# Optimization experiments

Measured on AMD Instinct MI355X. Metric: run time of the kernel, lower is better.

The kernel has to match this reference:

```python
import jax, jax.numpy as jnp
import numpy as np
from jax.scipy.special import logsumexp

EPSILON = 0.1
N_ITERS = 5


def setup_inputs() -> dict:
    key = jax.random.key(0)
    k1, k2, k3 = jax.random.split(key, 3)
    B, Q, T, D = 16, 1024, 1024, 256
    preds = jax.random.normal(k1, (B, Q, D), dtype=jnp.float32)
    targets = jax.random.normal(k2, (B, T, D), dtype=jnp.float32)
    filter = jax.random.normal(k3, (B, T), dtype=jnp.float32)
    return {"preds": preds, "targets": targets, "filter": filter}


def _cdist(x, y):
    x2 = jnp.sum(x * x, axis=-1)[:, :, None]          # [B,Q,1]
    y2 = jnp.sum(y * y, axis=-1)[:, None, :]          # [B,1,T]
    xy = jnp.einsum("bqd,btd->bqt", x, y)             # [B,Q,T]
    return jnp.sqrt(jnp.maximum(x2 + y2 - 2.0 * xy, 0.0))


def reference(preds, targets, filter):
    eps = EPSILON
    B, Q, _ = preds.shape
    T = targets.shape[1]
    cost = _cdist(preds, targets)                     # [B,Q,T]
    filter_cost = 2.0 * jnp.max(cost)
    cost = jnp.where(filter[:, None, :] <= 0, filter_cost, cost)
    u = jnp.zeros((B, Q), dtype=cost.dtype)
    v = jnp.zeros((B, T), dtype=cost.dtype)
    for _ in range(N_ITERS):
        u = -eps * logsumexp(-(cost - v[:, None, :]) / eps, axis=2)
        v = -eps * logsumexp(-(cost - u[:, :, None]) / eps, axis=1)
    P = jnp.exp((u[:, :, None] + v[:, None, :] - cost) / eps)
    idx_tgt = jnp.argmax(P, axis=2)
    return (idx_tgt, P)
```

## Files before the change

kernel.cpp:

```cpp
#include <hip/hip_runtime.h>
#include <math.h>

#define BB 16
#define QQ 1024
#define TT 1024
#define DD 256
#define EPS 0.1f
#define INV_EPS 10.0f
#define SINK_ITERS 5
#define FCONST 128.0f

typedef _Float16 f16;
typedef _Float16 f16x4 __attribute__((ext_vector_type(4)));
typedef _Float16 f16x8 __attribute__((ext_vector_type(8)));
typedef float f32x4 __attribute__((ext_vector_type(4)));

__global__ __launch_bounds__(256) void cvt_kernel(
    const float* __restrict__ preds, const float* __restrict__ targets,
    f16* __restrict__ Ahi, f16* __restrict__ Alo,
    f16* __restrict__ Bhi, f16* __restrict__ Blo,
    float* __restrict__ x2, float* __restrict__ y2)
{
  int w = threadIdx.x >> 6, l = threadIdx.x & 63;
  int row = blockIdx.x * 4 + w;
  const float* src; f16 *hi, *lo; float* nrm;
  if (row < BB*QQ) {
    src = preds + (size_t)row * DD;
    hi = Ahi + (size_t)row * DD; lo = Alo + (size_t)row * DD; nrm = x2 + row;
  } else {
    int r = row - BB*QQ;
    src = targets + (size_t)r * DD;
    hi = Bhi + (size_t)r * DD; lo = Blo + (size_t)r * DD; nrm = y2 + r;
  }
  float4 v = ((const float4*)src)[l];
  f16x4 h, lw;
  h.x = (f16)v.x; h.y = (f16)v.y; h.z = (f16)v.z; h.w = (f16)v.w;
  lw.x = (f16)(v.x - (float)h.x); lw.y = (f16)(v.y - (float)h.y);
  lw.z = (f16)(v.z - (float)h.z); lw.w = (f16)(v.w - (float)h.w);
  *(f16x4*)(hi + l*4) = h;
  *(f16x4*)(lo + l*4) = lw;
  float s = v.x*v.x + v.y*v.y + v.z*v.z + v.w*v.w;
  #pragma unroll
  for (int o = 32; o; o >>= 1) s += __shfl_down(s, o, 64);
  if (l == 0) *nrm = s;
}

__global__ __launch_bounds__(256) void cost_mfma_kernel(
    const f16* __restrict__ Ahi, const f16* __restrict__ Alo,
    const f16* __restrict__ Bhi, const f16* __restrict__ Blo,
    const float* __restrict__ x2, const float* __restrict__ y2,
    const float* __restrict__ filter,
    float* __restrict__ cost, float* __restrict__ costT, int useT)
{
  __shared__ f16 sA[2][128*32];
  __shared__ f16 sB[2][128*32];
  int b = blockIdx.z;
  int q0 = blockIdx.y * 128, t0 = blockIdx.x * 128;
  int tid = threadIdx.x, w = tid >> 6, l = tid & 63;
  int rq = (w >> 1) * 64, rt = (w & 1) * 64;
  int fr = l & 15, fg = l >> 4;
  const f16* pA[2] = { Ahi + ((size_t)b*QQ + q0) * DD, Alo + ((size_t)b*QQ + q0) * DD };
  const f16* pB[2] = { Bhi + ((size_t)b*TT + t0) * DD, Blo + ((size_t)b*TT + t0) * DD };
  f32x4 acc[4][4] = {};
  for (int k0 = 0; k0 < DD; k0 += 32) {
    __syncthreads();
#if __has_builtin(__builtin_amdgcn_global_load_lds)
    #pragma unroll
    for (int j = 0; j < 2; ++j) {
      int chunk = w*128 + j*64 + l;
      int row = chunk >> 2, kc = chunk & 3;
      size_t go = (size_t)row * DD + k0 + kc*8;
      int lb = (w*128 + j*64) * 8;
      #pragma unroll
      for (int h = 0; h < 2; ++h) {
        __builtin_amdgcn_global_load_lds(
            (const __attribute__((address_space(1))) void*)(pA[h] + go),
            (__attribute__((address_space(3))) void*)&sA[h][lb], 16, 0, 0);
        __builtin_amdgcn_global_load_lds(
            (const __attribute__((address_space(1))) void*)(pB[h] + go),
            (__attribute__((address_space(3))) void*)&sB[h][lb], 16, 0, 0);
      }
    }
#else
    #pragma unroll
    for (int j = 0; j < 2; ++j) {
      int chunk = w*128 + j*64 + l;
      int row = chunk >> 2, kc = chunk & 3;
      size_t go = (size_t)row * DD + k0 + kc*8;
      #pragma unroll
      for (int h = 0; h < 2; ++h) {
        *(f16x8*)&sA[h][chunk*8] = *(const f16x8*)(pA[h] + go);
        *(f16x8*)&sB[h][chunk*8] = *(const f16x8*)(pB[h] + go);
      }
    }
#endif
    __syncthreads();
    f16x8 ah[4], al[4], bh[4], bl[4];
    #pragma unroll
    for (int f = 0; f < 4; ++f) {
      int ao = (rq + f*16 + fr)*32 + fg*8;
      ah[f] = *(const f16x8*)&sA[0][ao];
      al[f] = *(const f16x8*)&sA[1][ao];
      int bo = (rt + f*16 + fr)*32 + fg*8;
      bh[f] = *(const f16x8*)&sB[0][bo];
      bl[f] = *(const f16x8*)&sB[1][bo];
    }
    #pragma unroll
    for (int fm = 0; fm < 4; ++fm)
      #pragma unroll
      for (int fn = 0; fn < 4; ++fn) {
        acc[fm][fn] = __builtin_amdgcn_mfma_f32_16x16x32_f16(ah[fm], bh[fn], acc[fm][fn], 0, 0, 0);
        acc[fm][fn] = __builtin_amdgcn_mfma_f32_16x16x32_f16(ah[fm], bl[fn], acc[fm][fn], 0, 0, 0);
        acc[fm][fn] = __builtin_amdgcn_mfma_f32_16x16x32_f16(al[fm], bh[fn], acc[fm][fn], 0, 0, 0);
      }
  }
  float xv[16];
  #pragma unroll
  for (int fm = 0; fm < 4; ++fm)
    #pragma unroll
    for (int r = 0; r < 4; ++r)
      xv[fm*4+r] = x2[(size_t)b*QQ + q0 + rq + fm*16 + fg*4 + r];
  float yv[4], fv[4];
  #pragma unroll
  for (int fn = 0; fn < 4; ++fn) {
    int t = t0 + rt + fn*16 + fr;
    yv[fn] = y2[(size_t)b*TT + t];
    fv[fn] = filter[(size_t)b*TT + t];
  }
  #pragma unroll
  for (int fm = 0; fm < 4; ++fm) {
    #pragma unroll
    for (int fn = 0; fn < 4; ++fn) {
      int t = t0 + rt + fn*16 + fr;
      float cvr[4];
      #pragma unroll
      for (int r = 0; r < 4; ++r) {
        float c2 = xv[fm*4+r] + yv[fn] - 2.0f*acc[fm][fn][r];
        float c = sqrtf(fmaxf(c2, 0.f));
        if (fv[fn] <= 0.f) c = FCONST;
        cvr[r] = c;
        int q = q0 + rq + fm*16 + fg*4 + r;
        cost[((size_t)b*QQ + q)*TT + t] = c;
      }
      if (useT) {
        float* dst = costT + ((size_t)b*TT + t)*QQ + q0 + rq + fm*16 + fg*4;
        *(float4*)dst = make_float4(cvr[0], cvr[1], cvr[2], cvr[3]);
      }
    }
  }
}

__global__ __launch_bounds__(64) void norms_kernel(
    const float* __restrict__ preds, const float* __restrict__ targets,
    float* __restrict__ x2, float* __restrict__ y2)
{
  int row = blockIdx.x;
  const float* src; float* dst;
  if (row < BB*QQ) { src = preds + (size_t)row * DD; dst = x2 + row; }
  else { int r = row - BB*QQ; src = targets + (size_t)r * DD; dst = y2 + r; }
  float4 v = ((const float4*)src)[threadIdx.x];
  float s = v.x*v.x + v.y*v.y + v.z*v.z + v.w*v.w;
  #pragma unroll
  for (int o = 32; o; o >>= 1) s += __shfl_down(s, o, 64);
  if (threadIdx.x == 0) *dst = s;
}

#define LDSTR 132
__global__ __launch_bounds__(256) void cost_fp32_kernel(
    const float* __restrict__ preds, const float* __restrict__ targets,
    const float* __restrict__ x2, const float* __restrict__ y2,
    const float* __restrict__ filter,
    float* __restrict__ cost, float* __restrict__ costT, int useT)
{
  __shared__ float As[16*LDSTR];
  __shared__ float Bs[16*LDSTR];
  int b  = blockIdx.z;
  int q0 = blockIdx.y * 128;
  int t0 = blockIdx.x * 128;
  const float* Ab = preds   + ((size_t)b*QQ + q0) * DD;
  const float* Bb = targets + ((size_t)b*TT + t0) * DD;
  int tid = threadIdx.x;
  int srow = tid >> 2, sq = (tid & 3) << 2;
  int w = tid >> 6, l = tid & 63;
  int rq = ((w >> 1) << 6) + ((l >> 3) << 3);
  int rt = ((w & 1) << 6) + ((l & 7) << 3);
  float acc[8][8] = {};
  for (int k0 = 0; k0 < DD; k0 += 16) {
    float4 a0 = *(const float4*)(Ab + (size_t)srow*DD + k0 + sq);
    float4 a1 = *(const float4*)(Ab + (size_t)(srow+64)*DD + k0 + sq);
    float4 b0 = *(const float4*)(Bb + (size_t)srow*DD + k0 + sq);
    float4 b1 = *(const float4*)(Bb + (size_t)(srow+64)*DD + k0 + sq);
    __syncthreads();
    As[(sq+0)*LDSTR + srow] = a0.x; As[(sq+1)*LDSTR + srow] = a0.y;
    As[(sq+2)*LDSTR + srow] = a0.z; As[(sq+3)*LDSTR + srow] = a0.w;
    As[(sq+0)*LDSTR + srow+64] = a1.x; As[(sq+1)*LDSTR + srow+64] = a1.y;
    As[(sq+2)*LDSTR + srow+64] = a1.z; As[(sq+3)*LDSTR + srow+64] = a1.w;
    Bs[(sq+0)*LDSTR + srow] = b0.x; Bs[(sq+1)*LDSTR + srow] = b0.y;
    Bs[(sq+2)*LDSTR + srow] = b0.z; Bs[(sq+3)*LDSTR + srow] = b0.w;
    Bs[(sq+0)*LDSTR + srow+64] = b1.x; Bs[(sq+1)*LDSTR + srow+64] = b1.y;
    Bs[(sq+2)*LDSTR + srow+64] = b1.z; Bs[(sq+3)*LDSTR + srow+64] = b1.w;
    __syncthreads();
    #pragma unroll
    for (int k = 0; k < 16; ++k) {
      float4 af0 = *(const float4*)&As[k*LDSTR + rq];
      float4 af1 = *(const float4*)&As[k*LDSTR + rq + 4];
      float4 bf0 = *(const float4*)&Bs[k*LDSTR + rt];
      float4 bf1 = *(const float4*)&Bs[k*LDSTR + rt + 4];
      float aa[8] = {af0.x,af0.y,af0.z,af0.w,af1.x,af1.y,af1.z,af1.w};
      float bb[8] = {bf0.x,bf0.y,bf0.z,bf0.w,bf1.x,bf1.y,bf1.z,bf1.w};
      #pragma unroll
      for (int i = 0; i < 8; ++i)
        #pragma unroll
        for (int j = 0; j < 8; ++j)
          acc[i][j] = fmaf(aa[i], bb[j], acc[i][j]);
    }
  }
  float xq[8], yt[8], fvv[8];
  #pragma unroll
  for (int i = 0; i < 8; ++i) xq[i] = x2[(size_t)b*QQ + q0 + rq + i];
  #pragma unroll
  for (int j = 0; j < 8; ++j) {
    yt[j] = y2[(size_t)b*TT + t0 + rt + j];
    fvv[j] = filter[(size_t)b*TT + t0 + rt + j];
  }
  float cv[8][8];
  #pragma unroll
  for (int i = 0; i < 8; ++i)
    #pragma unroll
    for (int j = 0; j < 8; ++j) {
      float c2 = xq[i] + yt[j] - 2.f*acc[i][j];
      float c = sqrtf(fmaxf(c2, 0.f));
      if (fvv[j] <= 0.f) c = FCONST;
      cv[i][j] = c;
    }
  #pragma unroll
  for (int i = 0; i < 8; ++i) {
    float* dst = cost + ((size_t)b*QQ + q0 + rq + i) * TT + t0 + rt;
    *(float4*)dst       = make_float4(cv[i][0], cv[i][1], cv[i][2], cv[i][3]);
    *(float4*)(dst + 4) = make_float4(cv[i][4], cv[i][5], cv[i][6], cv[i][7]);
  }
  if (useT) {
    #pragma unroll
    for (int j = 0; j < 8; ++j) {
      float* dst = costT + ((size_t)b*TT + t0 + rt + j) * QQ + q0 + rq;
      *(float4*)dst       = make_float4(cv[0][j], cv[1][j], cv[2][j], cv[3][j]);
      *(float4*)(dst + 4) = make_float4(cv[4][j], cv[5][j], cv[6][j], cv[7][j]);
    }
  }
}

__device__ __forceinline__ float wave_max64(float v) {
  #pragma unroll
  for (int o = 1; o < 64; o <<= 1) v = fmaxf(v, __shfl_xor(v, o, 64));
  return v;
}
__device__ __forceinline__ float wave_sum64(float v) {
  #pragma unroll
  for (int o = 1; o < 64; o <<= 1) v += __shfl_xor(v, o, 64);
  return v;
}

__global__ __launch_bounds__(256) void u_kernel(
    const float* __restrict__ cost, const float* __restrict__ v, float* __restrict__ u)
{
  int row = (blockIdx.x << 2) + (threadIdx.x >> 6);
  int l = threadIdx.x & 63;
  int b = row >> 10;
  const float4* cr = (const float4*)(cost + (size_t)row * TT);
  const float4* vb = (const float4*)(v + (size_t)b * TT);
  float s[16], m = -3.0e38f;
  #pragma unroll
  for (int i = 0; i < 4; ++i) {
    float4 c4 = cr[l + (i << 6)];
    float4 v4 = vb[l + (i << 6)];
    s[4*i+0] = (v4.x - c4.x) * INV_EPS;
    s[4*i+1] = (v4.y - c4.y) * INV_EPS;
    s[4*i+2] = (v4.z - c4.z) * INV_EPS;
    s[4*i+3] = (v4.w - c4.w) * INV_EPS;
    m = fmaxf(m, fmaxf(fmaxf(s[4*i+0], s[4*i+1]), fmaxf(s[4*i+2], s[4*i+3])));
  }
  m = wave_max64(m);
  float sum = 0.f;
  #pragma unroll
  for (int i = 0; i < 16; ++i) sum += expf(s[i] - m);
  sum = wave_sum64(sum);
  if (l == 0) u[row] = -EPS * (m + logf(sum));
}

__global__ __launch_bounds__(256) void v_kernel(
    const float* __restrict__ cost, const float* __restrict__ costT, int useT,
    const float* __restrict__ filter, const float* __restrict__ u, float* __restrict__ v)
{
  int row = (blockIdx.x << 2) + (threadIdx.x >> 6);
  int l = threadIdx.x & 63;
  int b = row >> 10;
  int t = row & 1023;
  const float4* ub = (const float4*)(u + (size_t)b * QQ);
  bool filt = (filter[row] <= 0.f);
  float s[16], m = -3.0e38f;
  if (filt) {
    #pragma unroll
    for (int i = 0; i < 4; ++i) {
      float4 u4 = ub[l + (i << 6)];
      s[4*i+0] = (u4.x - FCONST) * INV_EPS;
      s[4*i+1] = (u4.y - FCONST) * INV_EPS;
      s[4*i+2] = (u4.z - FCONST) * INV_EPS;
      s[4*i+3] = (u4.w - FCONST) * INV_EPS;
      m = fmaxf(m, fmaxf(fmaxf(s[4*i+0], s[4*i+1]), fmaxf(s[4*i+2], s[4*i+3])));
    }
  } else if (useT) {
    const float4* cr = (const float4*)(costT + (size_t)row * QQ);
    #pragma unroll
    for (int i = 0; i < 4; ++i) {
      float4 u4 = ub[l + (i << 6)];
      float4 c4 = cr[l + (i << 6)];
      s[4*i+0] = (u4.x - c4.x) * INV_EPS;
      s[4*i+1] = (u4.y - c4.y) * INV_EPS;
      s[4*i+2] = (u4.z - c4.z) * INV_EPS;
      s[4*i+3] = (u4.w - c4.w) * INV_EPS;
      m = fmaxf(m, fmaxf(fmaxf(s[4*i+0], s[4*i+1]), fmaxf(s[4*i+2], s[4*i+3])));
    }
  } else {
    const float* cr = cost + (size_t)b*QQ*TT + t;
    #pragma unroll
    for (int i = 0; i < 4; ++i) {
      float4 u4 = ub[l + (i << 6)];
      int q = (l + (i << 6)) << 2;
      float c0 = cr[(size_t)(q+0) * TT];
      float c1 = cr[(size_t)(q+1) * TT];
      float c2 = cr[(size_t)(q+2) * TT];
      float c3 = cr[(size_t)(q+3) * TT];
      s[4*i+0] = (u4.x - c0) * INV_EPS;
      s[4*i+1] = (u4.y - c1) * INV_EPS;
      s[4*i+2] = (u4.z - c2) * INV_EPS;
      s[4*i+3] = (u4.w - c3) * INV_EPS;
      m = fmaxf(m, fmaxf(fmaxf(s[4*i+0], s[4*i+1]), fmaxf(s[4*i+2], s[4*i+3])));
    }
  }
  m = wave_max64(m);
  float sum = 0.f;
  #pragma unroll
  for (int i = 0; i < 16; ++i) sum += expf(s[i] - m);
  sum = wave_sum64(sum);
  if (l == 0) v[row] = -EPS * (m + logf(sum));
}

__global__ __launch_bounds__(256) void p_kernel(
    float* __restrict__ P, const float* __restrict__ u, const float* __restrict__ v,
    float* __restrict__ idxOut)
{
  int row = (blockIdx.x << 2) + (threadIdx.x >> 6);
  int l = threadIdx.x & 63;
  int b = row >> 10;
  float4* cr = (float4*)(P + (size_t)row * TT);
  const float4* vb = (const float4*)(v + (size_t)b * TT);
  float uu = u[row];
  float bestp = -1.f; int bestt = 0;
  #pragma unroll
  for (int i = 0; i < 4; ++i) {
    float4 c4 = cr[l + (i << 6)];
    float4 v4 = vb[l + (i << 6)];
    int t0 = (l + (i << 6)) << 2;
    float4 p4;
    p4.x = expf((uu + v4.x - c4.x) * INV_EPS);
    p4.y = expf((uu + v4.y - c4.y) * INV_EPS);
    p4.z = expf((uu + v4.z - c4.z) * INV_EPS);
    p4.w = expf((uu + v4.w - c4.w) * INV_EPS);
    if (p4.x > bestp) { bestp = p4.x; bestt = t0 + 0; }
    if (p4.y > bestp) { bestp = p4.y; bestt = t0 + 1; }
    if (p4.z > bestp) { bestp = p4.z; bestt = t0 + 2; }
    if (p4.w > bestp) { bestp = p4.w; bestt = t0 + 3; }
    cr[l + (i << 6)] = p4;
  }
  #pragma unroll
  for (int o = 1; o < 64; o <<= 1) {
    float op = __shfl_xor(bestp, o, 64);
    int   ot = __shfl_xor(bestt, o, 64);
    if (op > bestp || (op == bestp && ot < bestt)) { bestp = op; bestt = ot; }
  }
  if (l == 0) idxOut[row] = (float)bestt;
}

extern "C" void kernel_launch(void* const* d_in, const int* in_sizes, int n_in,
                              void* d_out, int out_size, void* d_ws, size_t ws_size,
                              hipStream_t stream) {
  const float* preds   = (const float*)d_in[0];
  const float* targets = (const float*)d_in[1];
  const float* filter  = (const float*)d_in[2];
  float* out = (float*)d_out;
  float* idxOut = out;
  float* P = out + (size_t)BB*QQ;

  const size_t F16A  = (size_t)BB*QQ*DD;
  const size_t f16tot = 4 * F16A * sizeof(f16);
  const size_t smallb = (size_t)4 * 16384 * sizeof(float);
  const size_t costTB = (size_t)BB * QQ * TT * sizeof(float);

  char* p = (char*)d_ws;
  int useF16 = ws_size >= f16tot + smallb;
  f16 *Ahi, *Alo, *Bhi, *Blo;
  float *x2, *y2, *u, *v, *costT;
  int useT;
  if (useF16) {
    Ahi = (f16*)p; Alo = Ahi + F16A; Bhi = Alo + F16A; Blo = Bhi + F16A;
    x2 = (float*)(p + f16tot); y2 = x2 + 16384; u = y2 + 16384; v = u + 16384;
    useT = ws_size >= f16tot + smallb + costTB;
    costT = (float*)(p + f16tot + smallb);
  } else {
    Ahi = Alo = Bhi = Blo = nullptr;
    x2 = (float*)p; y2 = x2 + 16384; u = y2 + 16384; v = u + 16384;
    useT = ws_size >= smallb + costTB;
    costT = (float*)(p + smallb);
  }

  hipMemsetAsync(u, 0, (size_t)2 * 16384 * sizeof(float), stream);

  dim3 cg(TT/128, QQ/128, BB);
  if (useF16) {
    cvt_kernel<<<BB*(QQ+TT)/4, 256, 0, stream>>>(preds, targets, Ahi, Alo, Bhi, Blo, x2, y2);
    cost_mfma_kernel<<<cg, 256, 0, stream>>>(Ahi, Alo, Bhi, Blo, x2, y2, filter, P, costT, useT);
  } else {
    norms_kernel<<<BB*(QQ+TT), 64, 0, stream>>>(preds, targets, x2, y2);
    cost_fp32_kernel<<<cg, 256, 0, stream>>>(preds, targets, x2, y2, filter, P, costT, useT);
  }
  int rows_q = BB*QQ/4, rows_t = BB*TT/4;
  for (int it = 0; it < SINK_ITERS; ++it) {
    u_kernel<<<rows_q, 256, 0, stream>>>(P, v, u);
    v_kernel<<<rows_t, 256, 0, stream>>>(P, costT, useT, filter, u, v);
  }
  p_kernel<<<rows_q, 256, 0, stream>>>(P, u, v, idxOut);
}
```

Baseline: 286.9 us.

## Process two rows per wave, use native exp2/log2, skip costT writes for filtered columns

The u, v and p kernels now handle two rows per wavefront. This shares the v/u vector loads, raises memory-level parallelism and halves the block count. The exp/log calls become hardware exp2/log2 builtins, with the constants rescaled by log2(e), which cuts transcendental instruction cost. The cost kernels no longer write transposed cost rows for filtered target columns, since v_kernel never reads those rows. That saves a significant share of the transposed-store bandwidth, at the price of slightly reduced accuracy from the approximate builtins.

```diff
diff --git a/kernel.cpp b/kernel.cpp
--- a/kernel.cpp
+++ b/kernel.cpp
@@ -6,14 +6,30 @@
 #define TT 1024
 #define DD 256
 #define EPS 0.1f
-#define INV_EPS 10.0f
 #define SINK_ITERS 5
 #define FCONST 128.0f
+#define K2 14.426950408889634f
+#define EPSLN2 0.069314718055994531f
 
 typedef _Float16 f16;
 typedef _Float16 f16x4 __attribute__((ext_vector_type(4)));
 typedef _Float16 f16x8 __attribute__((ext_vector_type(8)));
 typedef float f32x4 __attribute__((ext_vector_type(4)));
+
+__device__ __forceinline__ float fast_exp2(float x) {
+#if __has_builtin(__builtin_amdgcn_exp2f)
+  return __builtin_amdgcn_exp2f(x);
+#else
+  return exp2f(x);
+#endif
+}
+__device__ __forceinline__ float fast_log2(float x) {
+#if __has_builtin(__builtin_amdgcn_logf)
+  return __builtin_amdgcn_logf(x);
+#else
+  return log2f(x);
+#endif
+}
 
 __global__ __launch_bounds__(256) void cvt_kernel(
     const float* __restrict__ preds, const float* __restrict__ targets,
@@ -142,7 +158,7 @@
         int q = q0 + rq + fm*16 + fg*4 + r;
         cost[((size_t)b*QQ + q)*TT + t] = c;
       }
-      if (useT) {
+      if (useT && fv[fn] > 0.f) {
         float* dst = costT + ((size_t)b*TT + t)*QQ + q0 + rq + fm*16 + fg*4;
         *(float4*)dst = make_float4(cvr[0], cvr[1], cvr[2], cvr[3]);
       }
@@ -242,6 +258,7 @@
   if (useT) {
     #pragma unroll
     for (int j = 0; j < 8; ++j) {
+      if (fvv[j] <= 0.f) continue;
       float* dst = costT + ((size_t)b*TT + t0 + rt + j) * QQ + q0 + rq;
       *(float4*)dst       = make_float4(cv[0][j], cv[1][j], cv[2][j], cv[3][j]);
       *(float4*)(dst + 4) = make_float4(cv[4][j], cv[5][j], cv[6][j], cv[7][j]);
@@ -263,122 +280,161 @@
 __global__ __launch_bounds__(256) void u_kernel(
     const float* __restrict__ cost, const float* __restrict__ v, float* __restrict__ u)
 {
-  int row = (blockIdx.x << 2) + (threadIdx.x >> 6);
-  int l = threadIdx.x & 63;
+  int w = threadIdx.x >> 6, l = threadIdx.x & 63;
+  int row = blockIdx.x * 8 + w * 2;
   int b = row >> 10;
-  const float4* cr = (const float4*)(cost + (size_t)row * TT);
+  const float4* c0 = (const float4*)(cost + (size_t)row * TT);
+  const float4* c1 = c0 + TT/4;
   const float4* vb = (const float4*)(v + (size_t)b * TT);
-  float s[16], m = -3.0e38f;
+  float s0[16], s1[16], m0 = -3.0e38f, m1 = -3.0e38f;
   #pragma unroll
   for (int i = 0; i < 4; ++i) {
-    float4 c4 = cr[l + (i << 6)];
     float4 v4 = vb[l + (i << 6)];
-    s[4*i+0] = (v4.x - c4.x) * INV_EPS;
-    s[4*i+1] = (v4.y - c4.y) * INV_EPS;
-    s[4*i+2] = (v4.z - c4.z) * INV_EPS;
-    s[4*i+3] = (v4.w - c4.w) * INV_EPS;
-    m = fmaxf(m, fmaxf(fmaxf(s[4*i+0], s[4*i+1]), fmaxf(s[4*i+2], s[4*i+3])));
-  }
-  m = wave_max64(m);
-  float sum = 0.f;
-  #pragma unroll
-  for (int i = 0; i < 16; ++i) sum += expf(s[i] - m);
-  sum = wave_sum64(sum);
-  if (l == 0) u[row] = -EPS * (m + logf(sum));
+    float4 a4 = c0[l + (i << 6)];
+    float4 b4 = c1[l + (i << 6)];
+    s0[4*i+0] = (v4.x - a4.x) * K2; s0[4*i+1] = (v4.y - a4.y) * K2;
+    s0[4*i+2] = (v4.z - a4.z) * K2; s0[4*i+3] = (v4.w - a4.w) * K2;
+    s1[4*i+0] = (v4.x - b4.x) * K2; s1[4*i+1] = (v4.y - b4.y) * K2;
+    s1[4*i+2] = (v4.z - b4.z) * K2; s1[4*i+3] = (v4.w - b4.w) * K2;
+    m0 = fmaxf(m0, fmaxf(fmaxf(s0[4*i+0], s0[4*i+1]), fmaxf(s0[4*i+2], s0[4*i+3])));
+    m1 = fmaxf(m1, fmaxf(fmaxf(s1[4*i+0], s1[4*i+1]), fmaxf(s1[4*i+2], s1[4*i+3])));
+  }
+  m0 = wave_max64(m0); m1 = wave_max64(m1);
+  float q0 = 0.f, q1 = 0.f;
+  #pragma unroll
+  for (int i = 0; i < 16; ++i) { q0 += fast_exp2(s0[i] - m0); q1 += fast_exp2(s1[i] - m1); }
+  q0 = wave_sum64(q0); q1 = wave_sum64(q1);
+  if (l == 0) {
+    u[row]   = -EPSLN2 * (m0 + fast_log2(q0));
+    u[row+1] = -EPSLN2 * (m1 + fast_log2(q1));
+  }
 }
 
 __global__ __launch_bounds__(256) void v_kernel(
     const float* __restrict__ cost, const float* __restrict__ costT, int useT,
     const float* __restrict__ filter, const float* __restrict__ u, float* __restrict__ v)
 {
-  int row = (blockIdx.x << 2) + (threadIdx.x >> 6);
-  int l = threadIdx.x & 63;
-  int b = row >> 10;
-  int t = row & 1023;
+  int w = threadIdx.x >> 6, l = threadIdx.x & 63;
+  int row = blockIdx.x * 8 + w * 2;
+  int b = row >> 10, t = row & 1023;
   const float4* ub = (const float4*)(u + (size_t)b * QQ);
-  bool filt = (filter[row] <= 0.f);
-  float s[16], m = -3.0e38f;
-  if (filt) {
-    #pragma unroll
-    for (int i = 0; i < 4; ++i) {
-      float4 u4 = ub[l + (i << 6)];
-      s[4*i+0] = (u4.x - FCONST) * INV_EPS;
-      s[4*i+1] = (u4.y - FCONST) * INV_EPS;
-      s[4*i+2] = (u4.z - FCONST) * INV_EPS;
-      s[4*i+3] = (u4.w - FCONST) * INV_EPS;
-      m = fmaxf(m, fmaxf(fmaxf(s[4*i+0], s[4*i+1]), fmaxf(s[4*i+2], s[4*i+3])));
+  bool f0 = (filter[row]   <= 0.f);
+  bool f1 = (filter[row+1] <= 0.f);
+  float4 uw[4];
+  #pragma unroll
+  for (int i = 0; i < 4; ++i) uw[i] = ub[l + (i << 6)];
+  float s0[16], s1[16], m0 = -3.0e38f, m1 = -3.0e38f;
+  if (f0) {
+    #pragma unroll
+    for (int i = 0; i < 4; ++i) {
+      s0[4*i+0] = (uw[i].x - FCONST) * K2; s0[4*i+1] = (uw[i].y - FCONST) * K2;
+      s0[4*i+2] = (uw[i].z - FCONST) * K2; s0[4*i+3] = (uw[i].w - FCONST) * K2;
     }
   } else if (useT) {
     const float4* cr = (const float4*)(costT + (size_t)row * QQ);
     #pragma unroll
     for (int i = 0; i < 4; ++i) {
-      float4 u4 = ub[l + (i << 6)];
       float4 c4 = cr[l + (i << 6)];
-      s[4*i+0] = (u4.x - c4.x) * INV_EPS;
-      s[4*i+1] = (u4.y - c4.y) * INV_EPS;
-      s[4*i+2] = (u4.z - c4.z) * INV_EPS;
-      s[4*i+3] = (u4.w - c4.w) * INV_EPS;
-      m = fmaxf(m, fmaxf(fmaxf(s[4*i+0], s[4*i+1]), fmaxf(s[4*i+2], s[4*i+3])));
+      s0[4*i+0] = (uw[i].x - c4.x) * K2; s0[4*i+1] = (uw[i].y - c4.y) * K2;
+      s0[4*i+2] = (uw[i].z - c4.z) * K2; s0[4*i+3] = (uw[i].w - c4.w) * K2;
     }
   } else {
     const float* cr = cost + (size_t)b*QQ*TT + t;
     #pragma unroll
     for (int i = 0; i < 4; ++i) {
-      float4 u4 = ub[l + (i << 6)];
       int q = (l + (i << 6)) << 2;
-      float c0 = cr[(size_t)(q+0) * TT];
-      float c1 = cr[(size_t)(q+1) * TT];
-      float c2 = cr[(size_t)(q+2) * TT];
-      float c3 = cr[(size_t)(q+3) * TT];
-      s[4*i+0] = (u4.x - c0) * INV_EPS;
-      s[4*i+1] = (u4.y - c1) * INV_EPS;
-      s[4*i+2] = (u4.z - c2) * INV_EPS;
-      s[4*i+3] = (u4.w - c3) * INV_EPS;
-      m = fmaxf(m, fmaxf(fmaxf(s[4*i+0], s[4*i+1]), fmaxf(s[4*i+2], s[4*i+3])));
-    }
-  }
-  m = wave_max64(m);
-  float sum = 0.f;
-  #pragma unroll
-  for (int i = 0; i < 16; ++i) sum += expf(s[i] - m);
-  sum = wave_sum64(sum);
-  if (l == 0) v[row] = -EPS * (m + logf(sum));
+      s0[4*i+0] = (uw[i].x - cr[(size_t)(q+0)*TT]) * K2;
+      s0[4*i+1] = (uw[i].y - cr[(size_t)(q+1)*TT]) * K2;
+      s0[4*i+2] = (uw[i].z - cr[(size_t)(q+2)*TT]) * K2;
+      s0[4*i+3] = (uw[i].w - cr[(size_t)(q+3)*TT]) * K2;
+    }
+  }
+  if (f1) {
+    #pragma unroll
+    for (int i = 0; i < 4; ++i) {
+      s1[4*i+0] = (uw[i].x - FCONST) * K2; s1[4*i+1] = (uw[i].y - FCONST) * K2;
+      s1[4*i+2] = (uw[i].z - FCONST) * K2; s1[4*i+3] = (uw[i].w - FCONST) * K2;
+    }
+  } else if (useT) {
+    const float4* cr = (const float4*)(costT + (size_t)(row+1) * QQ);
+    #pragma unroll
+    for (int i = 0; i < 4; ++i) {
+      float4 c4 = cr[l + (i << 6)];
+      s1[4*i+0] = (uw[i].x - c4.x) * K2; s1[4*i+1] = (uw[i].y - c4.y) * K2;
+      s1[4*i+2] = (uw[i].z - c4.z) * K2; s1[4*i+3] = (uw[i].w - c4.w) * K2;
+    }
+  } else {
+    const float* cr = cost + (size_t)b*QQ*TT + t + 1;
+    #pragma unroll
+    for (int i = 0; i < 4; ++i) {
+      int q = (l + (i << 6)) << 2;
+      s1[4*i+0] = (uw[i].x - cr[(size_t)(q+0)*TT]) * K2;
+      s1[4*i+1] = (uw[i].y - cr[(size_t)(q+1)*TT]) * K2;
+      s1[4*i+2] = (uw[i].z - cr[(size_t)(q+2)*TT]) * K2;
+      s1[4*i+3] = (uw[i].w - cr[(size_t)(q+3)*TT]) * K2;
+    }
+  }
+  #pragma unroll
+  for (int i = 0; i < 16; ++i) { m0 = fmaxf(m0, s0[i]); m1 = fmaxf(m1, s1[i]); }
+  m0 = wave_max64(m0); m1 = wave_max64(m1);
+  float q0 = 0.f, q1 = 0.f;
+  #pragma unroll
+  for (int i = 0; i < 16; ++i) { q0 += fast_exp2(s0[i] - m0); q1 += fast_exp2(s1[i] - m1); }
+  q0 = wave_sum64(q0); q1 = wave_sum64(q1);
+  if (l == 0) {
+    v[row]   = -EPSLN2 * (m0 + fast_log2(q0));
+    v[row+1] = -EPSLN2 * (m1 + fast_log2(q1));
+  }
 }
 
 __global__ __launch_bounds__(256) void p_kernel(
     float* __restrict__ P, const float* __restrict__ u, const float* __restrict__ v,
     float* __restrict__ idxOut)
 {
-  int row = (blockIdx.x << 2) + (threadIdx.x >> 6);
-  int l = threadIdx.x & 63;
+  int w = threadIdx.x >> 6, l = threadIdx.x & 63;
+  int row = blockIdx.x * 8 + w * 2;
   int b = row >> 10;
-  float4* cr = (float4*)(P + (size_t)row * TT);
+  float4* c0 = (float4*)(P + (size_t)row * TT);
+  float4* c1 = c0 + TT/4;
   const float4* vb = (const float4*)(v + (size_t)b * TT);
-  float uu = u[row];
-  float bestp = -1.f; int bestt = 0;
+  float u0 = u[row], u1 = u[row+1];
+  float bp0 = -1.f, bp1 = -1.f; int bt0 = 0, bt1 = 0;
   #pragma unroll
   for (int i = 0; i < 4; ++i) {
-    float4 c4 = cr[l + (i << 6)];
     float4 v4 = vb[l + (i << 6)];
+    float4 a4 = c0[l + (i << 6)];
+    float4 b4 = c1[l + (i << 6)];
     int t0 = (l + (i << 6)) << 2;
-    float4 p4;
-    p4.x = expf((uu + v4.x - c4.x) * INV_EPS);
-    p4.y = expf((uu + v4.y - c4.y) * INV_EPS);
-    p4.z = expf((uu + v4.z - c4.z) * INV_EPS);
-    p4.w = expf((uu + v4.w - c4.w) * INV_EPS);
-    if (p4.x > bestp) { bestp = p4.x; bestt = t0 + 0; }
-    if (p4.y > bestp) { bestp = p4.y; bestt = t0 + 1; }
-    if (p4.z > bestp) { bestp = p4.z; bestt = t0 + 2; }
-    if (p4.w > bestp) { bestp = p4.w; bestt = t0 + 3; }
-    cr[l + (i << 6)] = p4;
+    float4 p0, p1;
+    p0.x = fast_exp2((u0 + v4.x - a4.x) * K2);
+    p0.y = fast_exp2((u0 + v4.y - a4.y) * K2);
+    p0.z = fast_exp2((u0 + v4.z - a4.z) * K2);
+    p0.w = fast_exp2((u0 + v4.w - a4.w) * K2);
+    p1.x = fast_exp2((u1 + v4.x - b4.x) * K2);
+    p1.y = fast_exp2((u1 + v4.y - b4.y) * K2);
+    p1.z = fast_exp2((u1 + v4.z - b4.z) * K2);
+    p1.w = fast_exp2((u1 + v4.w - b4.w) * K2);
+    if (p0.x > bp0) { bp0 = p0.x; bt0 = t0 + 0; }
+    if (p0.y > bp0) { bp0 = p0.y; bt0 = t0 + 1; }
+    if (p0.z > bp0) { bp0 = p0.z; bt0 = t0 + 2; }
+    if (p0.w > bp0) { bp0 = p0.w; bt0 = t0 + 3; }
+    if (p1.x > bp1) { bp1 = p1.x; bt1 = t0 + 0; }
+    if (p1.y > bp1) { bp1 = p1.y; bt1 = t0 + 1; }
+    if (p1.z > bp1) { bp1 = p1.z; bt1 = t0 + 2; }
+    if (p1.w > bp1) { bp1 = p1.w; bt1 = t0 + 3; }
+    c0[l + (i << 6)] = p0;
+    c1[l + (i << 6)] = p1;
   }
   #pragma unroll
   for (int o = 1; o < 64; o <<= 1) {
-    float op = __shfl_xor(bestp, o, 64);
-    int   ot = __shfl_xor(bestt, o, 64);
-    if (op > bestp || (op == bestp && ot < bestt)) { bestp = op; bestt = ot; }
-  }
-  if (l == 0) idxOut[row] = (float)bestt;
+    float op = __shfl_xor(bp0, o, 64);
+    int   ot = __shfl_xor(bt0, o, 64);
+    if (op > bp0 || (op == bp0 && ot < bt0)) { bp0 = op; bt0 = ot; }
+    op = __shfl_xor(bp1, o, 64);
+    ot = __shfl_xor(bt1, o, 64);
+    if (op > bp1 || (op == bp1 && ot < bt1)) { bp1 = op; bt1 = ot; }
+  }
+  if (l == 0) { idxOut[row] = (float)bt0; idxOut[row+1] = (float)bt1; }
 }
 
 extern "C" void kernel_launch(void* const* d_in, const int* in_sizes, int n_in,
@@ -423,10 +479,10 @@
     norms_kernel<<<BB*(QQ+TT), 64, 0, stream>>>(preds, targets, x2, y2);
     cost_fp32_kernel<<<cg, 256, 0, stream>>>(preds, targets, x2, y2, filter, P, costT, useT);
   }
-  int rows_q = BB*QQ/4, rows_t = BB*TT/4;
+  int blks = BB*QQ/8;
   for (int it = 0; it < SINK_ITERS; ++it) {
-    u_kernel<<<rows_q, 256, 0, stream>>>(P, v, u);
-    v_kernel<<<rows_t, 256, 0, stream>>>(P, costT, useT, filter, u, v);
-  }
-  p_kernel<<<rows_q, 256, 0, stream>>>(P, u, v, idxOut);
-}
+    u_kernel<<<blks, 256, 0, stream>>>(P, v, u);
+    v_kernel<<<blks, 256, 0, stream>>>(P, costT, useT, filter, u, v);
+  }
+  p_kernel<<<blks, 256, 0, stream>>>(P, u, v, idxOut);
+}
```

Result: faster. 263.6 us (-8.1%).
